# Kernel optimization log

Hardware: AMD Instinct MI355X
Metric: run time of the kernel (lower is better)

The kernel has to match this reference:

```python
import jax, jax.numpy as jnp
import numpy as np

B, S, H = 4, 4096, 1024
E, K, DE, DS = 8, 2, 128, 512  # n_routed_experts, top_k, routed hidden, shared hidden


def setup_inputs() -> dict:
    key = jax.random.key(0)
    ks = jax.random.split(key, 10)
    sc = 0.02
    return {
        "x": jax.random.normal(ks[0], (B, S, H), dtype=jnp.float32),
        "Wg": jax.random.normal(ks[1], (E, H), dtype=jnp.float32) * sc,
        "W1": jax.random.normal(ks[2], (E, DE, H), dtype=jnp.float32) * sc,
        "b1": jnp.zeros((E, DE), dtype=jnp.float32),
        "W2": jax.random.normal(ks[3], (E, H, DE), dtype=jnp.float32) * sc,
        "b2": jnp.zeros((E, H), dtype=jnp.float32),
        "Ws1": jax.random.normal(ks[4], (DS, H), dtype=jnp.float32) * sc,
        "bs1": jnp.zeros((DS,), dtype=jnp.float32),
        "Ws2": jax.random.normal(ks[5], (H, DS), dtype=jnp.float32) * sc,
        "bs2": jnp.zeros((H,), dtype=jnp.float32),
    }


def reference(x, Wg, W1, b1, W2, b2, Ws1, bs1, Ws2, bs2):
    # FFNMoE forward, eval mode (dropout = identity, aux loss inactive).
    xf = x.reshape(-1, H)  # [T, H]
    # --- MOEGate: softmax scoring + top-k + normalized weights ---
    logits = xf @ Wg.T                         # [T, E]
    scores = jax.nn.softmax(logits, axis=-1)
    topk_w, topk_idx = jax.lax.top_k(scores, K)  # [T, K]
    topk_w = topk_w / (jnp.sum(topk_w, axis=-1, keepdims=True) + 1e-20)
    # Dense per-(token, expert) combine weight (topk indices are distinct).
    w = jnp.sum(jax.nn.one_hot(topk_idx, E, dtype=xf.dtype) * topk_w[..., None], axis=1)  # [T, E]
    # --- Routed experts: fc1 -> relu -> fc2, weighted scatter-combine ---
    h1 = jax.nn.relu(jnp.einsum('th,efh->tef', xf, W1) + b1)       # [T, E, DE]
    y = jnp.einsum('tef,ehf,te->th', h1, W2, w) + w @ b2           # [T, H]
    # --- Shared expert ---
    sh = jax.nn.relu(xf @ Ws1.T + bs1) @ Ws2.T + bs2               # [T, H]
    return (y + sh).reshape(x.shape)
```

## Files before the change

### kernel.cpp

```cpp
#include <hip/hip_runtime.h>
#include <cstdint>

#define TTOK 16384
#define HD   1024
#define NE   8
#define NDE  128
#define NDS  512
#define NC1  1536
#define KC2  1536

typedef float  f32x4  __attribute__((ext_vector_type(4)));
typedef __bf16 bf16x8 __attribute__((ext_vector_type(8)));

__device__ __forceinline__ unsigned short f2bf(float f) {
  unsigned int u = __float_as_uint(f);
  u += 0x7fffu + ((u >> 16) & 1u);
  return (unsigned short)(u >> 16);
}

__device__ __forceinline__ void gl2lds16(const void* gp, void* lp) {
  void* g0 = const_cast<void*>(gp);
  __builtin_amdgcn_global_load_lds((__attribute__((address_space(1))) void*)g0,
                                   (__attribute__((address_space(3))) void*)lp,
                                   16, 0, 0);
}

__global__ void prep_kernel(const float* __restrict__ W1, const float* __restrict__ Ws1,
                            const float* __restrict__ W2, const float* __restrict__ Ws2,
                            const float* __restrict__ b1, const float* __restrict__ bs1,
                            unsigned short* __restrict__ W1cat,
                            unsigned short* __restrict__ W2cat,
                            float* __restrict__ bias1) {
  const int total = NC1 * HD + HD * KC2 + NC1;
  for (int idx = blockIdx.x * 256 + threadIdx.x; idx < total; idx += gridDim.x * 256) {
    if (idx < NC1 * HD) {
      int r = idx >> 10, k = idx & 1023;
      float v = (r < 1024) ? W1[idx] : Ws1[(size_t)(r - 1024) * HD + k];
      W1cat[idx] = f2bf(v);
    } else if (idx < NC1 * HD + HD * KC2) {
      int i2 = idx - NC1 * HD;
      int h = i2 / KC2;
      int j = i2 - h * KC2;
      float v = (j < 1024) ? W2[(size_t)((j >> 7) * HD + h) * NDE + (j & 127)]
                           : Ws2[(size_t)h * NDS + (j - 1024)];
      W2cat[i2] = f2bf(v);
    } else {
      int r = idx - (NC1 * HD + HD * KC2);
      bias1[r] = (r < 1024) ? b1[r] : bs1[r - 1024];
    }
  }
}

__global__ __launch_bounds__(256) void gate_kernel(const float* __restrict__ x,
                                                   const float* __restrict__ Wg,
                                                   unsigned short* __restrict__ xbf,
                                                   float* __restrict__ wgt) {
  const int lane = threadIdx.x & 63;
  const int wv   = threadIdx.x >> 6;
  const int t    = blockIdx.x * 4 + wv;

  const float* xr = x + (size_t)t * HD + lane * 16;
  float4 x0 = ((const float4*)xr)[0];
  float4 x1 = ((const float4*)xr)[1];
  float4 x2 = ((const float4*)xr)[2];
  float4 x3 = ((const float4*)xr)[3];

  unsigned short* xo = xbf + (size_t)t * HD + lane * 16;
  union { unsigned short us[8]; uint4 v; } pk;
  pk.us[0] = f2bf(x0.x); pk.us[1] = f2bf(x0.y); pk.us[2] = f2bf(x0.z); pk.us[3] = f2bf(x0.w);
  pk.us[4] = f2bf(x1.x); pk.us[5] = f2bf(x1.y); pk.us[6] = f2bf(x1.z); pk.us[7] = f2bf(x1.w);
  ((uint4*)xo)[0] = pk.v;
  pk.us[0] = f2bf(x2.x); pk.us[1] = f2bf(x2.y); pk.us[2] = f2bf(x2.z); pk.us[3] = f2bf(x2.w);
  pk.us[4] = f2bf(x3.x); pk.us[5] = f2bf(x3.y); pk.us[6] = f2bf(x3.z); pk.us[7] = f2bf(x3.w);
  ((uint4*)xo)[1] = pk.v;

  float lg[8];
#pragma unroll
  for (int e = 0; e < 8; ++e) {
    const float4* wr = (const float4*)(Wg + (size_t)e * HD + lane * 16);
    float4 a = wr[0], b = wr[1], c = wr[2], d = wr[3];
    lg[e] = a.x * x0.x + a.y * x0.y + a.z * x0.z + a.w * x0.w +
            b.x * x1.x + b.y * x1.y + b.z * x1.z + b.w * x1.w +
            c.x * x2.x + c.y * x2.y + c.z * x2.z + c.w * x2.w +
            d.x * x3.x + d.y * x3.y + d.z * x3.z + d.w * x3.w;
  }
#pragma unroll
  for (int off = 32; off > 0; off >>= 1) {
#pragma unroll
    for (int e = 0; e < 8; ++e) lg[e] += __shfl_xor(lg[e], off, 64);
  }

  if (lane == 0) {
    int i1 = 0; float m1 = lg[0];
#pragma unroll
    for (int e = 1; e < 8; ++e) { if (lg[e] > m1) { m1 = lg[e]; i1 = e; } }
    int i2 = -1; float m2 = -3.4e38f;
#pragma unroll
    for (int e = 0; e < 8; ++e) { if (e != i1 && lg[e] > m2) { m2 = lg[e]; i2 = e; } }
    float Z = 0.f;
#pragma unroll
    for (int e = 0; e < 8; ++e) Z += expf(lg[e] - m1);
    float s1 = 1.f / Z;
    float s2 = expf(m2 - m1) / Z;
    float dn = s1 + s2 + 1e-20f;
    float w1 = s1 / dn, w2 = s2 / dn;
#pragma unroll
    for (int e = 0; e < 8; ++e) {
      float v = 0.f;
      if (e == i1) v = w1;
      if (e == i2) v = w2;
      wgt[(size_t)t * 8 + e] = v;
    }
  }
}

template <int MODE, int NTN>
__global__ __launch_bounds__(256) void moe_gemm(const unsigned short* __restrict__ A,
                                                const unsigned short* __restrict__ Bt,
                                                const float* __restrict__ wgt,
                                                const float* __restrict__ bias1,
                                                const float* __restrict__ b2,
                                                const float* __restrict__ bs2,
                                                unsigned short* __restrict__ outH,
                                                float* __restrict__ outY,
                                                int K) {
  __shared__ __align__(16) unsigned short As[128 * 64];
  __shared__ __align__(16) unsigned short Bs[128 * 64];

  const int tid   = threadIdx.x;
  const int lane  = tid & 63;
  const int wv    = tid >> 6;
  const int wm    = wv >> 1;
  const int wn    = wv & 1;
  const int r16   = lane & 15;
  const int quad  = lane >> 4;

  const int L    = blockIdx.x;
  const int xcd  = L & 7;
  const int slot = L >> 3;
  const int mg   = slot / NTN;
  const int nn   = slot - mg * NTN;
  const int tileM = (xcd + (mg << 3)) << 7;
  const int tileN = nn << 7;

  const unsigned short* gA[4];
  const unsigned short* gB[4];
  unsigned short* lA[4];
  unsigned short* lB[4];
#pragma unroll
  for (int i = 0; i < 4; ++i) {
    int idx = i * 256 + tid;
    int row = idx >> 3;
    int c   = idx & 7;
    int gcg = c ^ (row & 7);
    gA[i] = A + (size_t)(tileM + row) * K + gcg * 8;
    gB[i] = Bt + (size_t)(tileN + row) * K + gcg * 8;
    lA[i] = As + idx * 8;
    lB[i] = Bs + idx * 8;
  }

  int aoff[4], boff[4];
#pragma unroll
  for (int i = 0; i < 4; ++i) {
    int ra = wm * 64 + i * 16 + r16;
    aoff[i] = ra * 64 + ((quad ^ (ra & 7)) << 3);
    int rb = wn * 64 + i * 16 + r16;
    boff[i] = rb * 64 + ((quad ^ (rb & 7)) << 3);
  }

  f32x4 acc[4][4];
#pragma unroll
  for (int i = 0; i < 4; ++i)
#pragma unroll
    for (int j = 0; j < 4; ++j) acc[i][j] = (f32x4){0.f, 0.f, 0.f, 0.f};

  const int nkt = K >> 6;
  for (int kt = 0; kt < nkt; ++kt) {
    const int ko = kt << 6;
#pragma unroll
    for (int i = 0; i < 4; ++i) gl2lds16(gA[i] + ko, lA[i]);
#pragma unroll
    for (int i = 0; i < 4; ++i) gl2lds16(gB[i] + ko, lB[i]);
    __syncthreads();

#pragma unroll
    for (int g = 0; g < 2; ++g) {
      const int gx = g << 5;
      bf16x8 av[4], bv[4];
#pragma unroll
      for (int i = 0; i < 4; ++i) av[i] = *(const bf16x8*)(As + (aoff[i] ^ gx));
#pragma unroll
      for (int j = 0; j < 4; ++j) bv[j] = *(const bf16x8*)(Bs + (boff[j] ^ gx));
#pragma unroll
      for (int i = 0; i < 4; ++i)
#pragma unroll
        for (int j = 0; j < 4; ++j)
          acc[i][j] = __builtin_amdgcn_mfma_f32_16x16x32_bf16(av[i], bv[j], acc[i][j], 0, 0, 0);
    }
    __syncthreads();
  }

  if (MODE == 0) {
    float* wl = (float*)As;
    const bool routed = (tileN < 1024);
    if (routed && tid < 128) wl[tid] = wgt[(size_t)(tileM + tid) * 8 + (tileN >> 7)];
    __syncthreads();
#pragma unroll
    for (int j = 0; j < 4; ++j) {
      const int col = tileN + wn * 64 + j * 16 + r16;
      const float bz = bias1[col];
#pragma unroll
      for (int i = 0; i < 4; ++i) {
#pragma unroll
        for (int r = 0; r < 4; ++r) {
          const int lrow = wm * 64 + i * 16 + quad * 4 + r;
          float v = acc[i][j][r] + bz;
          v = fmaxf(v, 0.f);
          if (routed) v *= wl[lrow];
          outH[(size_t)(tileM + lrow) * NC1 + col] = f2bf(v);
        }
      }
    }
  } else {
    float* wl = (float*)As;
    for (int idx = tid; idx < 128 * 8; idx += 256) {
      int rr = idx >> 3, ee = idx & 7;
      wl[rr * 9 + ee] = wgt[(size_t)tileM * 8 + idx];
    }
    __syncthreads();
    float b2c[4][8], bsc[4];
#pragma unroll
    for (int j = 0; j < 4; ++j) {
      const int col = tileN + wn * 64 + j * 16 + r16;
      bsc[j] = bs2[col];
#pragma unroll
      for (int e = 0; e < 8; ++e) b2c[j][e] = b2[(size_t)e * HD + col];
    }
#pragma unroll
    for (int i = 0; i < 4; ++i) {
#pragma unroll
      for (int r = 0; r < 4; ++r) {
        const int lrow = wm * 64 + i * 16 + quad * 4 + r;
        float w8[8];
#pragma unroll
        for (int e = 0; e < 8; ++e) w8[e] = wl[lrow * 9 + e];
#pragma unroll
        for (int j = 0; j < 4; ++j) {
          const int col = tileN + wn * 64 + j * 16 + r16;
          float v = acc[i][j][r] + bsc[j];
#pragma unroll
          for (int e = 0; e < 8; ++e) v += w8[e] * b2c[j][e];
          outY[(size_t)(tileM + lrow) * HD + col] = v;
        }
      }
    }
  }
}

extern "C" void kernel_launch(void* const* d_in, const int* in_sizes, int n_in,
                              void* d_out, int out_size, void* d_ws, size_t ws_size,
                              hipStream_t stream) {
  const float* x   = (const float*)d_in[0];
  const float* Wg  = (const float*)d_in[1];
  const float* W1  = (const float*)d_in[2];
  const float* b1  = (const float*)d_in[3];
  const float* W2  = (const float*)d_in[4];
  const float* b2  = (const float*)d_in[5];
  const float* Ws1 = (const float*)d_in[6];
  const float* bs1 = (const float*)d_in[7];
  const float* Ws2 = (const float*)d_in[8];
  const float* bs2 = (const float*)d_in[9];

  char* ws = (char*)d_ws;
  size_t off = 0;
  unsigned short* xbf   = (unsigned short*)(ws + off); off += (size_t)TTOK * HD * 2;
  unsigned short* Hcat  = (unsigned short*)(ws + off); off += (size_t)TTOK * NC1 * 2;
  unsigned short* W1cat = (unsigned short*)(ws + off); off += (size_t)NC1 * HD * 2;
  unsigned short* W2cat = (unsigned short*)(ws + off); off += (size_t)HD * KC2 * 2;
  float* wgt            = (float*)(ws + off);          off += (size_t)TTOK * 8 * 4;
  float* bias1          = (float*)(ws + off);          off += (size_t)NC1 * 4;

  prep_kernel<<<3080, 256, 0, stream>>>(W1, Ws1, W2, Ws2, b1, bs1, W1cat, W2cat, bias1);
  gate_kernel<<<TTOK / 4, 256, 0, stream>>>(x, Wg, xbf, wgt);
  moe_gemm<0, NC1 / 128><<<NC1 / 128 * TTOK / 128, 256, 0, stream>>>(
      xbf, W1cat, wgt, bias1, nullptr, nullptr, Hcat, nullptr, HD);
  moe_gemm<1, HD / 128><<<HD / 128 * TTOK / 128, 256, 0, stream>>>(
      Hcat, W2cat, wgt, nullptr, b2, bs2, nullptr, (float*)d_out, KC2);
}
```

Baseline: 304.6 us.

## Group tokens by expert pair and run sparse fc1/fc2 over routed tiles

The dense compute over all 8 experts becomes sparse routing. Tokens are bucketed by their top-2 expert pair (28 pairs) using atomic counters in the gate. A scan kernel builds a permutation and a tile table, and the fc1 and fc2 GEMMs then compute only the two selected experts plus the shared expert per tile, gathering and scattering rows by token. This cuts GEMM work from 1536-wide to 768-wide hidden layers, at the cost of an extra kernel, a memset, gather/scatter indirection, padded partial tiles, and a MAXT tile cap that could overflow if the routing is very skewed. Weight prep and gating are also merged into a single launch.

After: 330.7 us. 1.09x slower.

```diff
diff --git a/kernel.cpp b/kernel.cpp
--- a/kernel.cpp
+++ b/kernel.cpp
@@ -8,6 +8,11 @@
 #define NDS  512
 #define NC1  1536
 #define KC2  1536
+#define NPAIR 28
+#define MAXT  160
+#define PREPB 3080
+#define GATEB 4096
+#define NH    768
 
 typedef float  f32x4  __attribute__((ext_vector_type(4)));
 typedef __bf16 bf16x8 __attribute__((ext_vector_type(8)));
@@ -25,39 +30,38 @@
                                    16, 0, 0);
 }
 
-__global__ void prep_kernel(const float* __restrict__ W1, const float* __restrict__ Ws1,
-                            const float* __restrict__ W2, const float* __restrict__ Ws2,
-                            const float* __restrict__ b1, const float* __restrict__ bs1,
-                            unsigned short* __restrict__ W1cat,
-                            unsigned short* __restrict__ W2cat,
-                            float* __restrict__ bias1) {
-  const int total = NC1 * HD + HD * KC2 + NC1;
-  for (int idx = blockIdx.x * 256 + threadIdx.x; idx < total; idx += gridDim.x * 256) {
-    if (idx < NC1 * HD) {
-      int r = idx >> 10, k = idx & 1023;
-      float v = (r < 1024) ? W1[idx] : Ws1[(size_t)(r - 1024) * HD + k];
-      W1cat[idx] = f2bf(v);
-    } else if (idx < NC1 * HD + HD * KC2) {
-      int i2 = idx - NC1 * HD;
-      int h = i2 / KC2;
-      int j = i2 - h * KC2;
-      float v = (j < 1024) ? W2[(size_t)((j >> 7) * HD + h) * NDE + (j & 127)]
-                           : Ws2[(size_t)h * NDS + (j - 1024)];
-      W2cat[i2] = f2bf(v);
-    } else {
-      int r = idx - (NC1 * HD + HD * KC2);
-      bias1[r] = (r < 1024) ? b1[r] : bs1[r - 1024];
+__global__ __launch_bounds__(256) void prep_gate(
+    const float* __restrict__ x, const float* __restrict__ Wg,
+    const float* __restrict__ W1, const float* __restrict__ Ws1,
+    const float* __restrict__ W2, const float* __restrict__ Ws2,
+    const float* __restrict__ b1, const float* __restrict__ bs1,
+    unsigned short* __restrict__ W1cat, unsigned short* __restrict__ W2cat,
+    float* __restrict__ bias1, unsigned short* __restrict__ xbf,
+    float2* __restrict__ wpair, int* __restrict__ prank, int* __restrict__ cnt) {
+  if (blockIdx.x < PREPB) {
+    const int total = NC1 * HD + HD * KC2 + NC1;
+    for (int idx = blockIdx.x * 256 + threadIdx.x; idx < total; idx += PREPB * 256) {
+      if (idx < NC1 * HD) {
+        int r = idx >> 10, k = idx & 1023;
+        float v = (r < 1024) ? W1[idx] : Ws1[(size_t)(r - 1024) * HD + k];
+        W1cat[idx] = f2bf(v);
+      } else if (idx < NC1 * HD + HD * KC2) {
+        int i2 = idx - NC1 * HD;
+        int h = i2 / KC2;
+        int j = i2 - h * KC2;
+        float v = (j < 1024) ? W2[(size_t)((j >> 7) * HD + h) * NDE + (j & 127)]
+                             : Ws2[(size_t)h * NDS + (j - 1024)];
+        W2cat[i2] = f2bf(v);
+      } else {
+        int r = idx - (NC1 * HD + HD * KC2);
+        bias1[r] = (r < 1024) ? b1[r] : bs1[r - 1024];
+      }
     }
-  }
-}
-
-__global__ __launch_bounds__(256) void gate_kernel(const float* __restrict__ x,
-                                                   const float* __restrict__ Wg,
-                                                   unsigned short* __restrict__ xbf,
-                                                   float* __restrict__ wgt) {
+    return;
+  }
   const int lane = threadIdx.x & 63;
   const int wv   = threadIdx.x >> 6;
-  const int t    = blockIdx.x * 4 + wv;
+  const int t    = (blockIdx.x - PREPB) * 4 + wv;
 
   const float* xr = x + (size_t)t * HD + lane * 16;
   float4 x0 = ((const float4*)xr)[0];
@@ -104,44 +108,75 @@
     float s2 = expf(m2 - m1) / Z;
     float dn = s1 + s2 + 1e-20f;
     float w1 = s1 / dn, w2 = s2 / dn;
-#pragma unroll
-    for (int e = 0; e < 8; ++e) {
-      float v = 0.f;
-      if (e == i1) v = w1;
-      if (e == i2) v = w2;
-      wgt[(size_t)t * 8 + e] = v;
-    }
-  }
-}
-
-template <int MODE, int NTN>
-__global__ __launch_bounds__(256) void moe_gemm(const unsigned short* __restrict__ A,
-                                                const unsigned short* __restrict__ Bt,
-                                                const float* __restrict__ wgt,
-                                                const float* __restrict__ bias1,
-                                                const float* __restrict__ b2,
-                                                const float* __restrict__ bs2,
-                                                unsigned short* __restrict__ outH,
-                                                float* __restrict__ outY,
-                                                int K) {
+    int ef, es; float wf, wsx;
+    if (i1 < i2) { ef = i1; es = i2; wf = w1; wsx = w2; }
+    else         { ef = i2; es = i1; wf = w2; wsx = w1; }
+    int p = ef * 7 - (ef * (ef - 1)) / 2 + (es - ef - 1);
+    int rank = atomicAdd(&cnt[p], 1);
+    wpair[t] = make_float2(wf, wsx);
+    prank[t] = (p << 16) | rank;
+  }
+}
+
+__global__ __launch_bounds__(256) void route_scan(const int* __restrict__ cnt,
+                                                  const int* __restrict__ prank,
+                                                  int* __restrict__ perm,
+                                                  int4* __restrict__ tiletab,
+                                                  int* __restrict__ ntct) {
+  const int p = blockIdx.x;
+  int c[NPAIR];
+#pragma unroll
+  for (int q = 0; q < NPAIR; ++q) c[q] = cnt[q];
+  int estart = 0, tstart = 0;
+  for (int q = 0; q < p; ++q) { estart += c[q]; tstart += (c[q] + 127) >> 7; }
+  const int nt = (c[p] + 127) >> 7;
+  if (p == NPAIR - 1 && threadIdx.x == 0) ntct[0] = tstart + nt;
+  for (int k = threadIdx.x; k < nt; k += 256) {
+    int4 e;
+    e.x = p;
+    e.y = estart + (k << 7);
+    e.z = min(128, c[p] - (k << 7));
+    e.w = (tstart + k) << 7;
+    tiletab[tstart + k] = e;
+  }
+  for (int t = threadIdx.x; t < TTOK; t += 256) {
+    int v = prank[t];
+    if ((v >> 16) == p) perm[estart + (v & 0xffff)] = t;
+  }
+}
+
+__global__ __launch_bounds__(256) void moe_fc1(const unsigned short* __restrict__ xbf,
+                                               const unsigned short* __restrict__ W1cat,
+                                               const int* __restrict__ perm,
+                                               const float2* __restrict__ wpair,
+                                               const float* __restrict__ bias1,
+                                               const int4* __restrict__ tiletab,
+                                               const int* __restrict__ ntct,
+                                               unsigned short* __restrict__ Hbuf) {
+  const int L   = blockIdx.x;
+  const int xcd = L & 7;
+  const int s   = L >> 3;
+  const int mg  = s / 6;
+  const int nn  = s - mg * 6;
+  const int mt  = xcd + (mg << 3);
+  if (mt >= ntct[0]) return;
+  const int4 tt = tiletab[mt];
+  const int eoff = tt.y, valid = tt.z, hbase = tt.w;
+  int ef = 0, rem = tt.x;
+  while (rem >= 7 - ef) { rem -= 7 - ef; ef++; }
+  const int es = ef + 1 + rem;
+  const int brow = (nn == 0) ? ef * 128 : (nn == 1) ? es * 128 : 1024 + ((nn - 2) << 7);
+
   __shared__ __align__(16) unsigned short As[128 * 64];
   __shared__ __align__(16) unsigned short Bs[128 * 64];
 
-  const int tid   = threadIdx.x;
-  const int lane  = tid & 63;
-  const int wv    = tid >> 6;
-  const int wm    = wv >> 1;
-  const int wn    = wv & 1;
-  const int r16   = lane & 15;
-  const int quad  = lane >> 4;
-
-  const int L    = blockIdx.x;
-  const int xcd  = L & 7;
-  const int slot = L >> 3;
-  const int mg   = slot / NTN;
-  const int nn   = slot - mg * NTN;
-  const int tileM = (xcd + (mg << 3)) << 7;
-  const int tileN = nn << 7;
+  const int tid  = threadIdx.x;
+  const int lane = tid & 63;
+  const int wv   = tid >> 6;
+  const int wm   = wv >> 1;
+  const int wn   = wv & 1;
+  const int r16  = lane & 15;
+  const int quad = lane >> 4;
 
   const unsigned short* gA[4];
   const unsigned short* gB[4];
@@ -151,10 +186,11 @@
   for (int i = 0; i < 4; ++i) {
     int idx = i * 256 + tid;
     int row = idx >> 3;
-    int c   = idx & 7;
-    int gcg = c ^ (row & 7);
-    gA[i] = A + (size_t)(tileM + row) * K + gcg * 8;
-    gB[i] = Bt + (size_t)(tileN + row) * K + gcg * 8;
+    int cc  = idx & 7;
+    int kc  = cc ^ (row & 7);
+    int tok = perm[eoff + min(row, valid - 1)];
+    gA[i] = xbf + (size_t)tok * HD + kc * 8;
+    gB[i] = W1cat + (size_t)(brow + row) * HD + kc * 8;
     lA[i] = As + idx * 8;
     lB[i] = Bs + idx * 8;
   }
@@ -174,15 +210,13 @@
 #pragma unroll
     for (int j = 0; j < 4; ++j) acc[i][j] = (f32x4){0.f, 0.f, 0.f, 0.f};
 
-  const int nkt = K >> 6;
-  for (int kt = 0; kt < nkt; ++kt) {
+  for (int kt = 0; kt < 16; ++kt) {
     const int ko = kt << 6;
 #pragma unroll
     for (int i = 0; i < 4; ++i) gl2lds16(gA[i] + ko, lA[i]);
 #pragma unroll
     for (int i = 0; i < 4; ++i) gl2lds16(gB[i] + ko, lB[i]);
     __syncthreads();
-
 #pragma unroll
     for (int g = 0; g < 2; ++g) {
       const int gx = g << 5;
@@ -200,58 +234,151 @@
     __syncthreads();
   }
 
-  if (MODE == 0) {
-    float* wl = (float*)As;
-    const bool routed = (tileN < 1024);
-    if (routed && tid < 128) wl[tid] = wgt[(size_t)(tileM + tid) * 8 + (tileN >> 7)];
-    __syncthreads();
-#pragma unroll
-    for (int j = 0; j < 4; ++j) {
-      const int col = tileN + wn * 64 + j * 16 + r16;
-      const float bz = bias1[col];
-#pragma unroll
-      for (int i = 0; i < 4; ++i) {
-#pragma unroll
-        for (int r = 0; r < 4; ++r) {
-          const int lrow = wm * 64 + i * 16 + quad * 4 + r;
-          float v = acc[i][j][r] + bz;
-          v = fmaxf(v, 0.f);
-          if (routed) v *= wl[lrow];
-          outH[(size_t)(tileM + lrow) * NC1 + col] = f2bf(v);
-        }
+  float* wl = (float*)As;
+  if (tid < 128) {
+    int tok = perm[eoff + min(tid, valid - 1)];
+    float sc = 1.0f;
+    if (nn == 0) sc = wpair[tok].x;
+    else if (nn == 1) sc = wpair[tok].y;
+    wl[tid] = sc;
+  }
+  __syncthreads();
+#pragma unroll
+  for (int j = 0; j < 4; ++j) {
+    const int cin = wn * 64 + j * 16 + r16;
+    const float bz = bias1[brow + cin];
+#pragma unroll
+    for (int i = 0; i < 4; ++i) {
+#pragma unroll
+      for (int r = 0; r < 4; ++r) {
+        const int lrow = wm * 64 + i * 16 + quad * 4 + r;
+        float v = fmaxf(acc[i][j][r] + bz, 0.f) * wl[lrow];
+        Hbuf[(size_t)(hbase + lrow) * NH + nn * 128 + cin] = f2bf(v);
       }
     }
-  } else {
-    float* wl = (float*)As;
-    for (int idx = tid; idx < 128 * 8; idx += 256) {
-      int rr = idx >> 3, ee = idx & 7;
-      wl[rr * 9 + ee] = wgt[(size_t)tileM * 8 + idx];
+  }
+}
+
+__global__ __launch_bounds__(256) void moe_fc2(const unsigned short* __restrict__ Hbuf,
+                                               const unsigned short* __restrict__ W2cat,
+                                               const int* __restrict__ perm,
+                                               const float2* __restrict__ wpair,
+                                               const float* __restrict__ b2,
+                                               const float* __restrict__ bs2,
+                                               const int4* __restrict__ tiletab,
+                                               const int* __restrict__ ntct,
+                                               float* __restrict__ out) {
+  const int L   = blockIdx.x;
+  const int xcd = L & 7;
+  const int s   = L >> 3;
+  const int mg  = s >> 3;
+  const int nn  = s & 7;
+  const int mt  = xcd + (mg << 3);
+  if (mt >= ntct[0]) return;
+  const int4 tt = tiletab[mt];
+  const int eoff = tt.y, valid = tt.z, hbase = tt.w;
+  int ef = 0, rem = tt.x;
+  while (rem >= 7 - ef) { rem -= 7 - ef; ef++; }
+  const int es = ef + 1 + rem;
+  const int tileN = nn << 7;
+
+  __shared__ __align__(16) unsigned short As[128 * 64];
+  __shared__ __align__(16) unsigned short Bs[128 * 64];
+
+  const int tid  = threadIdx.x;
+  const int lane = tid & 63;
+  const int wv   = tid >> 6;
+  const int wm   = wv >> 1;
+  const int wn   = wv & 1;
+  const int r16  = lane & 15;
+  const int quad = lane >> 4;
+
+  const unsigned short* gA[4];
+  const unsigned short* gB[4];
+  unsigned short* lA[4];
+  unsigned short* lB[4];
+#pragma unroll
+  for (int i = 0; i < 4; ++i) {
+    int idx = i * 256 + tid;
+    int row = idx >> 3;
+    int cc  = idx & 7;
+    int kc  = cc ^ (row & 7);
+    gA[i] = Hbuf + (size_t)(hbase + row) * NH + kc * 8;
+    gB[i] = W2cat + (size_t)(tileN + row) * KC2 + kc * 8;
+    lA[i] = As + idx * 8;
+    lB[i] = Bs + idx * 8;
+  }
+
+  int aoff[4], boff[4];
+#pragma unroll
+  for (int i = 0; i < 4; ++i) {
+    int ra = wm * 64 + i * 16 + r16;
+    aoff[i] = ra * 64 + ((quad ^ (ra & 7)) << 3);
+    int rb = wn * 64 + i * 16 + r16;
+    boff[i] = rb * 64 + ((quad ^ (rb & 7)) << 3);
+  }
+
+  f32x4 acc[4][4];
+#pragma unroll
+  for (int i = 0; i < 4; ++i)
+#pragma unroll
+    for (int j = 0; j < 4; ++j) acc[i][j] = (f32x4){0.f, 0.f, 0.f, 0.f};
+
+  for (int kt = 0; kt < 12; ++kt) {
+    const int koA = kt << 6;
+    const int koB = (kt < 2) ? ef * 128 + (kt << 6)
+                 : (kt < 4) ? es * 128 + ((kt - 2) << 6)
+                            : 1024 + ((kt - 4) << 6);
+#pragma unroll
+    for (int i = 0; i < 4; ++i) gl2lds16(gA[i] + koA, lA[i]);
+#pragma unroll
+    for (int i = 0; i < 4; ++i) gl2lds16(gB[i] + koB, lB[i]);
+    __syncthreads();
+#pragma unroll
+    for (int g = 0; g < 2; ++g) {
+      const int gx = g << 5;
+      bf16x8 av[4], bv[4];
+#pragma unroll
+      for (int i = 0; i < 4; ++i) av[i] = *(const bf16x8*)(As + (aoff[i] ^ gx));
+#pragma unroll
+      for (int j = 0; j < 4; ++j) bv[j] = *(const bf16x8*)(Bs + (boff[j] ^ gx));
+#pragma unroll
+      for (int i = 0; i < 4; ++i)
+#pragma unroll
+        for (int j = 0; j < 4; ++j)
+          acc[i][j] = __builtin_amdgcn_mfma_f32_16x16x32_bf16(av[i], bv[j], acc[i][j], 0, 0, 0);
     }
     __syncthreads();
-    float b2c[4][8], bsc[4];
-#pragma unroll
-    for (int j = 0; j < 4; ++j) {
-      const int col = tileN + wn * 64 + j * 16 + r16;
-      bsc[j] = bs2[col];
-#pragma unroll
-      for (int e = 0; e < 8; ++e) b2c[j][e] = b2[(size_t)e * HD + col];
-    }
-#pragma unroll
-    for (int i = 0; i < 4; ++i) {
-#pragma unroll
-      for (int r = 0; r < 4; ++r) {
-        const int lrow = wm * 64 + i * 16 + quad * 4 + r;
-        float w8[8];
-#pragma unroll
-        for (int e = 0; e < 8; ++e) w8[e] = wl[lrow * 9 + e];
-#pragma unroll
-        for (int j = 0; j < 4; ++j) {
-          const int col = tileN + wn * 64 + j * 16 + r16;
-          float v = acc[i][j][r] + bsc[j];
-#pragma unroll
-          for (int e = 0; e < 8; ++e) v += w8[e] * b2c[j][e];
-          outY[(size_t)(tileM + lrow) * HD + col] = v;
-        }
+  }
+
+  float2* wl2 = (float2*)As;
+  int* tokl   = (int*)Bs;
+  if (tid < 128) {
+    int tokc = perm[eoff + min(tid, valid - 1)];
+    tokl[tid] = (tid < valid) ? tokc : -1;
+    wl2[tid] = wpair[tokc];
+  }
+  __syncthreads();
+  float bsc[4], b2a[4], b2b[4];
+#pragma unroll
+  for (int j = 0; j < 4; ++j) {
+    const int col = tileN + wn * 64 + j * 16 + r16;
+    bsc[j] = bs2[col];
+    b2a[j] = b2[(size_t)ef * HD + col];
+    b2b[j] = b2[(size_t)es * HD + col];
+  }
+#pragma unroll
+  for (int i = 0; i < 4; ++i) {
+#pragma unroll
+    for (int r = 0; r < 4; ++r) {
+      const int lrow = wm * 64 + i * 16 + quad * 4 + r;
+      const int tok = tokl[lrow];
+      if (tok < 0) continue;
+      const float2 w = wl2[lrow];
+#pragma unroll
+      for (int j = 0; j < 4; ++j) {
+        const int col = tileN + wn * 64 + j * 16 + r16;
+        out[(size_t)tok * HD + col] = acc[i][j][r] + bsc[j] + w.x * b2a[j] + w.y * b2b[j];
       }
     }
   }
@@ -274,16 +401,22 @@
   char* ws = (char*)d_ws;
   size_t off = 0;
   unsigned short* xbf   = (unsigned short*)(ws + off); off += (size_t)TTOK * HD * 2;
-  unsigned short* Hcat  = (unsigned short*)(ws + off); off += (size_t)TTOK * NC1 * 2;
+  unsigned short* Hbuf  = (unsigned short*)(ws + off); off += (size_t)MAXT * 128 * NH * 2;
   unsigned short* W1cat = (unsigned short*)(ws + off); off += (size_t)NC1 * HD * 2;
   unsigned short* W2cat = (unsigned short*)(ws + off); off += (size_t)HD * KC2 * 2;
-  float* wgt            = (float*)(ws + off);          off += (size_t)TTOK * 8 * 4;
   float* bias1          = (float*)(ws + off);          off += (size_t)NC1 * 4;
-
-  prep_kernel<<<3080, 256, 0, stream>>>(W1, Ws1, W2, Ws2, b1, bs1, W1cat, W2cat, bias1);
-  gate_kernel<<<TTOK / 4, 256, 0, stream>>>(x, Wg, xbf, wgt);
-  moe_gemm<0, NC1 / 128><<<NC1 / 128 * TTOK / 128, 256, 0, stream>>>(
-      xbf, W1cat, wgt, bias1, nullptr, nullptr, Hcat, nullptr, HD);
-  moe_gemm<1, HD / 128><<<HD / 128 * TTOK / 128, 256, 0, stream>>>(
-      Hcat, W2cat, wgt, nullptr, b2, bs2, nullptr, (float*)d_out, KC2);
-}
+  float2* wpair         = (float2*)(ws + off);         off += (size_t)TTOK * 8;
+  int* prank            = (int*)(ws + off);            off += (size_t)TTOK * 4;
+  int* perm             = (int*)(ws + off);            off += (size_t)TTOK * 4;
+  int4* tiletab         = (int4*)(ws + off);           off += (size_t)MAXT * 16;
+  int* cnt              = (int*)(ws + off);            off += 128;
+  int* ntct             = (int*)(ws + off);            off += 16;
+
+  hipMemsetAsync(cnt, 0, 128, stream);
+  prep_gate<<<PREPB + GATEB, 256, 0, stream>>>(x, Wg, W1, Ws1, W2, Ws2, b1, bs1,
+                                               W1cat, W2cat, bias1, xbf, wpair, prank, cnt);
+  route_scan<<<NPAIR, 256, 0, stream>>>(cnt, prank, perm, tiletab, ntct);
+  moe_fc1<<<8 * 20 * 6, 256, 0, stream>>>(xbf, W1cat, perm, wpair, bias1, tiletab, ntct, Hbuf);
+  moe_fc2<<<8 * 20 * 8, 256, 0, stream>>>(Hbuf, W2cat, perm, wpair, b2, bs2, tiletab, ntct,
+                                          (float*)d_out);
+}
```
